# Kernel tuning notes

Hardware: AMD Instinct MI355X
Metric: run time of the kernel (lower is better)

The kernel has to match this reference:

```python
import jax, jax.numpy as jnp
import numpy as np

D_MODEL = 1024
NUM_HEADS = 16
D_K = D_MODEL // NUM_HEADS
B, S = 2, 2048


def setup_inputs() -> dict:
    key = jax.random.key(0)
    ks = jax.random.split(key, 11)
    s = 1.0 / np.sqrt(D_MODEL)
    inp = {
        "Q": jax.random.normal(ks[0], (B, S, D_MODEL), jnp.float32),
        "K": jax.random.normal(ks[1], (B, S, D_MODEL), jnp.float32),
        "V": jax.random.normal(ks[2], (B, S, D_MODEL), jnp.float32),
        "Wq": jax.random.uniform(ks[3], (D_MODEL, D_MODEL), jnp.float32, -s, s),
        "bq": jax.random.uniform(ks[4], (D_MODEL,), jnp.float32, -s, s),
        "Wk": jax.random.uniform(ks[5], (D_MODEL, D_MODEL), jnp.float32, -s, s),
        "bk": jax.random.uniform(ks[6], (D_MODEL,), jnp.float32, -s, s),
        "Wv": jax.random.uniform(ks[7], (D_MODEL, D_MODEL), jnp.float32, -s, s),
        "bv": jax.random.uniform(ks[8], (D_MODEL,), jnp.float32, -s, s),
        "Wo": jax.random.uniform(ks[9], (D_MODEL, D_MODEL), jnp.float32, -s, s),
        "bo": jax.random.uniform(ks[10], (D_MODEL,), jnp.float32, -s, s),
    }
    return inp


def _split_heads(x):
    b, s, _ = x.shape
    return x.reshape(b, s, NUM_HEADS, D_K).transpose(0, 2, 1, 3)  # [B,H,S,Dk]


def reference(Q, K, V, Wq, bq, Wk, bk, Wv, bv, Wo, bo):
    q = _split_heads(Q @ Wq.T + bq)
    k = _split_heads(K @ Wk.T + bk)
    v = _split_heads(V @ Wv.T + bv)
    scale = 1.0 / jnp.sqrt(jnp.asarray(D_K, q.dtype))
    scores = jnp.einsum("bhqd,bhkd->bhqk", q, k) * scale  # [B,H,S,S]
    attn = jax.nn.softmax(scores, axis=-1)
    out = jnp.einsum("bhqk,bhkd->bhqd", attn, v)
    out = out.transpose(0, 2, 1, 3).reshape(Q.shape[0], -1, D_MODEL)
    return out @ Wo.T + bo
```

## Files before the change

kernel.cpp:

```cpp
#include <hip/hip_runtime.h>
#include <stdint.h>

typedef __bf16 bf16;
typedef __bf16 bf16x8 __attribute__((ext_vector_type(8)));
typedef float floatx4 __attribute__((ext_vector_type(4)));

#define S_LEN 2048
#define DM 1024
#define NH 16
#define DK 64
#define MTOT 4096

__device__ __forceinline__ void gll16(const void* g, void* l) {
  __builtin_amdgcn_global_load_lds(
      (const __attribute__((address_space(1))) void*)g,
      (__attribute__((address_space(3))) void*)l, 16, 0, 0);
}

__global__ __launch_bounds__(256) void cvt_w_kernel(
    const float* __restrict__ Wq, const float* __restrict__ Wk, const float* __restrict__ Wv,
    bf16* __restrict__ wqb, bf16* __restrict__ wkb, bf16* __restrict__ wvb)
{
  const int z = blockIdx.y;
  const float* src = (z == 0) ? Wq : (z == 1) ? Wk : Wv;
  bf16* dst = (z == 0) ? wqb : (z == 1) ? wkb : wvb;
  const int base = (blockIdx.x * 256 + threadIdx.x) * 8;
  float4 a = *(const float4*)(src + base);
  float4 b = *(const float4*)(src + base + 4);
  bf16x8 h;
  h[0] = (bf16)a.x; h[1] = (bf16)a.y; h[2] = (bf16)a.z; h[3] = (bf16)a.w;
  h[4] = (bf16)b.x; h[5] = (bf16)b.y; h[6] = (bf16)b.z; h[7] = (bf16)b.w;
  *(bf16x8*)(dst + base) = h;
}

__global__ __launch_bounds__(256) void proj_kernel(
    const float* __restrict__ Xq, const float* __restrict__ Xk, const float* __restrict__ Xv,
    const bf16* __restrict__ wqb, const bf16* __restrict__ wkb, const bf16* __restrict__ wvb,
    const float* __restrict__ bqp, const float* __restrict__ bkp, const float* __restrict__ bvp,
    bf16* __restrict__ qb, bf16* __restrict__ kb, bf16* __restrict__ vtb)
{
  const int z = blockIdx.z;
  const float* X    = (z == 0) ? Xq  : (z == 1) ? Xk  : Xv;
  const bf16* W     = (z == 0) ? wqb : (z == 1) ? wkb : wvb;
  const float* bias = (z == 0) ? bqp : (z == 1) ? bkp : bvp;

  const int m0 = blockIdx.x * 128;
  const int n0 = blockIdx.y * 128;
  const int tid = threadIdx.x;
  const int lane = tid & 63;
  const int wid = tid >> 6;
  const int wm = (wid & 1) * 64;
  const int wn = (wid >> 1) * 64;

  __shared__ float Asf[128 * 64];
  __shared__ bf16  Bs[128 * 64];

  floatx4 acc[4][4];
  #pragma unroll
  for (int i = 0; i < 4; i++)
    #pragma unroll
    for (int j = 0; j < 4; j++) acc[i][j] = (floatx4){0.f, 0.f, 0.f, 0.f};

  const int mr = lane & 15;
  const int q4 = lane >> 4;

  const int xrow_in = lane >> 4;
  const int xcb_ph  = lane & 15;
  const int wrow_in = lane >> 3;
  const int wcb_ph  = lane & 7;

  for (int kt = 0; kt < DM; kt += 64) {
    __syncthreads();
    #pragma unroll
    for (int j = 0; j < 8; j++) {
      const int c = wid * 8 + j;
      const int row = c * 4 + xrow_in;
      const int cb = xcb_ph ^ (row & 7);
      gll16(X + (size_t)(m0 + row) * DM + kt + cb * 4, &Asf[c * 256]);
    }
    #pragma unroll
    for (int j = 0; j < 4; j++) {
      const int c = wid * 4 + j;
      const int row = c * 8 + wrow_in;
      const int cb = wcb_ph ^ (row & 7);
      gll16(W + (size_t)(n0 + row) * DM + kt + cb * 8, &Bs[c * 512]);
    }
    __syncthreads();

    #pragma unroll
    for (int kk = 0; kk < 2; kk++) {
      bf16x8 af[4], bfr[4];
      #pragma unroll
      for (int mt = 0; mt < 4; mt++) {
        const int row = wm + mt * 16 + mr;
        const int cb0 = 8 * kk + 2 * q4;
        const float4 lo = *(const float4*)&Asf[row * 64 + (cb0 ^ (row & 7)) * 4];
        const float4 hi = *(const float4*)&Asf[row * 64 + ((cb0 + 1) ^ (row & 7)) * 4];
        bf16x8 a;
        a[0] = (bf16)lo.x; a[1] = (bf16)lo.y; a[2] = (bf16)lo.z; a[3] = (bf16)lo.w;
        a[4] = (bf16)hi.x; a[5] = (bf16)hi.y; a[6] = (bf16)hi.z; a[7] = (bf16)hi.w;
        af[mt] = a;
      }
      #pragma unroll
      for (int nt = 0; nt < 4; nt++) {
        const int row = wn + nt * 16 + mr;
        const int cb = 4 * kk + q4;
        bfr[nt] = *(const bf16x8*)&Bs[row * 64 + (cb ^ (row & 7)) * 8];
      }
      #pragma unroll
      for (int mt = 0; mt < 4; mt++)
        #pragma unroll
        for (int nt = 0; nt < 4; nt++)
          acc[mt][nt] = __builtin_amdgcn_mfma_f32_16x16x32_bf16(af[mt], bfr[nt], acc[mt][nt], 0, 0, 0);
    }
  }

  const float qscale = (z == 0) ? 0.125f : 1.0f;
  #pragma unroll
  for (int nt = 0; nt < 4; nt++) {
    const int gn = n0 + wn + nt * 16 + mr;
    const float bv = bias[gn];
    const int h = gn >> 6, d = gn & 63;
    #pragma unroll
    for (int mt = 0; mt < 4; mt++) {
      const int mbase = m0 + wm + mt * 16 + q4 * 4;
      #pragma unroll
      for (int r = 0; r < 4; r++) {
        const int gm = mbase + r;
        const int bi = gm >> 11, s = gm & 2047;
        const bf16 hv = (bf16)((acc[mt][nt][r] + bv) * qscale);
        if (z == 2) {
          vtb[(((size_t)(bi * NH + h)) * DK + d) * S_LEN + s] = hv;
        } else if (z == 0) {
          qb[(((size_t)(bi * NH + h)) * S_LEN + s) * DK + d] = hv;
        } else {
          kb[(((size_t)(bi * NH + h)) * S_LEN + s) * DK + d] = hv;
        }
      }
    }
  }
}

__global__ __launch_bounds__(256) void attn_kernel(
    const bf16* __restrict__ qb, const bf16* __restrict__ kb,
    const bf16* __restrict__ vtb, bf16* __restrict__ ob)
{
  const int qt = blockIdx.x;
  const int bh = blockIdx.y;
  const int tid = threadIdx.x;
  const int lane = tid & 63;
  const int wid = tid >> 6;

  const bf16* qh = qb + (size_t)bh * S_LEN * DK;
  const bf16* kh = kb + (size_t)bh * S_LEN * DK;
  const bf16* vh = vtb + (size_t)bh * DK * S_LEN;

  __shared__ bf16 Ks[128 * 64];
  __shared__ bf16 Vs[64 * 128];
  __shared__ bf16 Ps[4][16][136];

  const int mr = lane & 15;
  const int q4 = lane >> 4;
  const int k0 = q4 * 8;

  bf16x8 aq[2];
  #pragma unroll
  for (int kk = 0; kk < 2; kk++)
    aq[kk] = *(const bf16x8*)(qh + (size_t)(qt * 64 + wid * 16 + mr) * DK + kk * 32 + k0);

  floatx4 acc_o[4];
  #pragma unroll
  for (int i = 0; i < 4; i++) acc_o[i] = (floatx4){0.f, 0.f, 0.f, 0.f};
  float l_p[4] = {0.f, 0.f, 0.f, 0.f};

  const int krow_in = lane >> 3;
  const int kcb_ph  = lane & 7;
  const int vrow_in = lane >> 4;
  const int vcb_ph  = lane & 15;

  for (int it = 0; it < S_LEN / 128; it++) {
    const int s0 = it * 128;
    __syncthreads();
    #pragma unroll
    for (int j = 0; j < 4; j++) {
      const int c = wid * 4 + j;
      const int row = c * 8 + krow_in;
      const int cb = kcb_ph ^ (row & 7);
      gll16(kh + (size_t)(s0 + row) * DK + cb * 8, &Ks[c * 512]);
    }
    #pragma unroll
    for (int j = 0; j < 4; j++) {
      const int c = wid * 4 + j;
      const int row = c * 4 + vrow_in;
      const int cb = vcb_ph ^ (row & 7);
      gll16(vh + (size_t)row * S_LEN + s0 + cb * 8, &Vs[c * 512]);
    }
    __syncthreads();

    floatx4 sc[8];
    #pragma unroll
    for (int i = 0; i < 8; i++) sc[i] = (floatx4){0.f, 0.f, 0.f, 0.f};
    #pragma unroll
    for (int kk = 0; kk < 2; kk++) {
      #pragma unroll
      for (int nt = 0; nt < 8; nt++) {
        const int row = nt * 16 + mr;
        const int cb = kk * 4 + q4;
        bf16x8 b = *(const bf16x8*)&Ks[row * 64 + (cb ^ (row & 7)) * 8];
        sc[nt] = __builtin_amdgcn_mfma_f32_16x16x32_bf16(aq[kk], b, sc[nt], 0, 0, 0);
      }
    }

    #pragma unroll
    for (int nt = 0; nt < 8; nt++) {
      #pragma unroll
      for (int r = 0; r < 4; r++) {
        const float pv = __expf(sc[nt][r]);
        l_p[r] += pv;
        Ps[wid][q4 * 4 + r][nt * 16 + mr] = (bf16)pv;
      }
    }

    #pragma unroll
    for (int kk2 = 0; kk2 < 4; kk2++) {
      bf16x8 a = *(const bf16x8*)&Ps[wid][mr][kk2 * 32 + k0];
      #pragma unroll
      for (int dt = 0; dt < 4; dt++) {
        const int row = dt * 16 + mr;
        const int cb = kk2 * 4 + q4;
        bf16x8 b = *(const bf16x8*)&Vs[row * 128 + (cb ^ (row & 7)) * 8];
        acc_o[dt] = __builtin_amdgcn_mfma_f32_16x16x32_bf16(a, b, acc_o[dt], 0, 0, 0);
      }
    }
  }

  #pragma unroll
  for (int r = 0; r < 4; r++) {
    #pragma unroll
    for (int off = 1; off < 16; off <<= 1) l_p[r] += __shfl_xor(l_p[r], off, 16);
    l_p[r] = 1.0f / l_p[r];
  }

  const int bi = bh >> 4, h = bh & 15;
  #pragma unroll
  for (int dt = 0; dt < 4; dt++) {
    const int d = dt * 16 + mr;
    #pragma unroll
    for (int r = 0; r < 4; r++) {
      const int s = qt * 64 + wid * 16 + q4 * 4 + r;
      ob[((size_t)(bi * S_LEN + s)) * DM + h * DK + d] = (bf16)(acc_o[dt][r] * l_p[r]);
    }
  }
}

__global__ __launch_bounds__(256) void oproj_kernel(
    const bf16* __restrict__ X, const float* __restrict__ W,
    const float* __restrict__ bias, float* __restrict__ out)
{
  const int m0 = blockIdx.x * 128;
  const int n0 = blockIdx.y * 128;
  const int tid = threadIdx.x;
  const int lane = tid & 63;
  const int wid = tid >> 6;
  const int wm = (wid & 1) * 64;
  const int wn = (wid >> 1) * 64;

  __shared__ bf16  As[128 * 64];
  __shared__ float Bsf[128 * 64];

  floatx4 acc[4][4];
  #pragma unroll
  for (int i = 0; i < 4; i++)
    #pragma unroll
    for (int j = 0; j < 4; j++) acc[i][j] = (floatx4){0.f, 0.f, 0.f, 0.f};

  const int mr = lane & 15;
  const int q4 = lane >> 4;

  const int arow_in = lane >> 3;
  const int acb_ph  = lane & 7;
  const int brow_in = lane >> 4;
  const int bcb_ph  = lane & 15;

  for (int kt = 0; kt < DM; kt += 64) {
    __syncthreads();
    #pragma unroll
    for (int j = 0; j < 4; j++) {
      const int c = wid * 4 + j;
      const int row = c * 8 + arow_in;
      const int cb = acb_ph ^ (row & 7);
      gll16(X + (size_t)(m0 + row) * DM + kt + cb * 8, &As[c * 512]);
    }
    #pragma unroll
    for (int j = 0; j < 8; j++) {
      const int c = wid * 8 + j;
      const int row = c * 4 + brow_in;
      const int cb = bcb_ph ^ (row & 7);
      gll16(W + (size_t)(n0 + row) * DM + kt + cb * 4, &Bsf[c * 256]);
    }
    __syncthreads();

    #pragma unroll
    for (int kk = 0; kk < 2; kk++) {
      bf16x8 af[4], bfr[4];
      #pragma unroll
      for (int mt = 0; mt < 4; mt++) {
        const int row = wm + mt * 16 + mr;
        const int cb = 4 * kk + q4;
        af[mt] = *(const bf16x8*)&As[row * 64 + (cb ^ (row & 7)) * 8];
      }
      #pragma unroll
      for (int nt = 0; nt < 4; nt++) {
        const int row = wn + nt * 16 + mr;
        const int cb0 = 8 * kk + 2 * q4;
        const float4 lo = *(const float4*)&Bsf[row * 64 + (cb0 ^ (row & 7)) * 4];
        const float4 hi = *(const float4*)&Bsf[row * 64 + ((cb0 + 1) ^ (row & 7)) * 4];
        bf16x8 b;
        b[0] = (bf16)lo.x; b[1] = (bf16)lo.y; b[2] = (bf16)lo.z; b[3] = (bf16)lo.w;
        b[4] = (bf16)hi.x; b[5] = (bf16)hi.y; b[6] = (bf16)hi.z; b[7] = (bf16)hi.w;
        bfr[nt] = b;
      }
      #pragma unroll
      for (int mt = 0; mt < 4; mt++)
        #pragma unroll
        for (int nt = 0; nt < 4; nt++)
          acc[mt][nt] = __builtin_amdgcn_mfma_f32_16x16x32_bf16(af[mt], bfr[nt], acc[mt][nt], 0, 0, 0);
    }
  }

  #pragma unroll
  for (int nt = 0; nt < 4; nt++) {
    const int gn = n0 + wn + nt * 16 + mr;
    const float bv = bias[gn];
    #pragma unroll
    for (int mt = 0; mt < 4; mt++) {
      const int mbase = m0 + wm + mt * 16 + q4 * 4;
      #pragma unroll
      for (int r = 0; r < 4; r++)
        out[(size_t)(mbase + r) * DM + gn] = acc[mt][nt][r] + bv;
    }
  }
}

extern "C" void kernel_launch(void* const* d_in, const int* in_sizes, int n_in,
                              void* d_out, int out_size, void* d_ws, size_t ws_size,
                              hipStream_t stream) {
  const float* Q  = (const float*)d_in[0];
  const float* K  = (const float*)d_in[1];
  const float* V  = (const float*)d_in[2];
  const float* Wq = (const float*)d_in[3];
  const float* bq = (const float*)d_in[4];
  const float* Wk = (const float*)d_in[5];
  const float* bk = (const float*)d_in[6];
  const float* Wv = (const float*)d_in[7];
  const float* bv = (const float*)d_in[8];
  const float* Wo = (const float*)d_in[9];
  const float* bo = (const float*)d_in[10];
  float* out = (float*)d_out;

  const size_t NE = (size_t)MTOT * DM;
  bf16* qb  = (bf16*)d_ws;
  bf16* kb  = qb + NE;
  bf16* vtb = kb + NE;
  bf16* ao  = vtb + NE;
  bf16* wqb = ao;
  bf16* wkb = ao + (size_t)DM * DM;
  bf16* wvb = ao + 2 * (size_t)DM * DM;

  cvt_w_kernel<<<dim3(512, 3), 256, 0, stream>>>(Wq, Wk, Wv, wqb, wkb, wvb);
  proj_kernel<<<dim3(32, 8, 3), 256, 0, stream>>>(Q, K, V, wqb, wkb, wvb, bq, bk, bv, qb, kb, vtb);
  attn_kernel<<<dim3(32, 32), 256, 0, stream>>>(qb, kb, vtb, ao);
  oproj_kernel<<<dim3(32, 8), 256, 0, stream>>>(ao, Wo, bo, out);
}
```

Measured before the change: 282.8 us.

## Pre-convert Q/K inputs to bf16, double attention rows per warp, narrow oproj tiles

The conversion kernel now also casts the Q and K activations to bf16, staging them in the output buffer, so the Q and K projections load bf16 tiles instead of converting fp32 in LDS. The attention kernel now has each warp handle 32 query rows instead of 16, reusing each K and V LDS fragment for two MFMAs and halving the grid. The output projection uses 128x64 tiles, doubling its block count for better occupancy. The extra conversion pass adds global traffic, and the attention change raises register and LDS pressure.

```diff
diff --git a/kernel.cpp b/kernel.cpp
--- a/kernel.cpp
+++ b/kernel.cpp
@@ -17,14 +17,20 @@
       (__attribute__((address_space(3))) void*)l, 16, 0, 0);
 }
 
-__global__ __launch_bounds__(256) void cvt_w_kernel(
+__global__ __launch_bounds__(256) void cvt_kernel(
     const float* __restrict__ Wq, const float* __restrict__ Wk, const float* __restrict__ Wv,
-    bf16* __restrict__ wqb, bf16* __restrict__ wkb, bf16* __restrict__ wvb)
+    const float* __restrict__ Xq, const float* __restrict__ Xk,
+    bf16* __restrict__ wqb, bf16* __restrict__ wkb, bf16* __restrict__ wvb,
+    bf16* __restrict__ xqb, bf16* __restrict__ xkb)
 {
-  const int z = blockIdx.y;
-  const float* src = (z == 0) ? Wq : (z == 1) ? Wk : Wv;
-  bf16* dst = (z == 0) ? wqb : (z == 1) ? wkb : wvb;
-  const int base = (blockIdx.x * 256 + threadIdx.x) * 8;
+  const int c = blockIdx.x;
+  const float* src; bf16* dst; int off;
+  if      (c < 512)  { src = Wq; dst = wqb; off = c; }
+  else if (c < 1024) { src = Wk; dst = wkb; off = c - 512; }
+  else if (c < 1536) { src = Wv; dst = wvb; off = c - 1024; }
+  else if (c < 3584) { src = Xq; dst = xqb; off = c - 1536; }
+  else               { src = Xk; dst = xkb; off = c - 3584; }
+  const size_t base = (size_t)off * 2048 + threadIdx.x * 8;
   float4 a = *(const float4*)(src + base);
   float4 b = *(const float4*)(src + base + 4);
   bf16x8 h;
@@ -34,13 +40,12 @@
 }
 
 __global__ __launch_bounds__(256) void proj_kernel(
-    const float* __restrict__ Xq, const float* __restrict__ Xk, const float* __restrict__ Xv,
+    const bf16* __restrict__ xqb, const bf16* __restrict__ xkb, const float* __restrict__ Xv,
     const bf16* __restrict__ wqb, const bf16* __restrict__ wkb, const bf16* __restrict__ wvb,
     const float* __restrict__ bqp, const float* __restrict__ bkp, const float* __restrict__ bvp,
     bf16* __restrict__ qb, bf16* __restrict__ kb, bf16* __restrict__ vtb)
 {
   const int z = blockIdx.z;
-  const float* X    = (z == 0) ? Xq  : (z == 1) ? Xk  : Xv;
   const bf16* W     = (z == 0) ? wqb : (z == 1) ? wkb : wvb;
   const float* bias = (z == 0) ? bqp : (z == 1) ? bkp : bvp;
 
@@ -52,8 +57,10 @@
   const int wm = (wid & 1) * 64;
   const int wn = (wid >> 1) * 64;
 
-  __shared__ float Asf[128 * 64];
-  __shared__ bf16  Bs[128 * 64];
+  __shared__ unsigned char smemA[32768];
+  __shared__ bf16 Bs[128 * 64];
+  bf16*  As16 = (bf16*)smemA;
+  float* Asf  = (float*)smemA;
 
   floatx4 acc[4][4];
   #pragma unroll
@@ -64,25 +71,35 @@
   const int mr = lane & 15;
   const int q4 = lane >> 4;
 
-  const int xrow_in = lane >> 4;
-  const int xcb_ph  = lane & 15;
-  const int wrow_in = lane >> 3;
-  const int wcb_ph  = lane & 7;
+  const int r8_in = lane >> 3, cb8_ph = lane & 7;
+  const int r4_in = lane >> 4, cb16_ph = lane & 15;
+
+  const bf16* Xb = (z == 0) ? xqb : xkb;
 
   for (int kt = 0; kt < DM; kt += 64) {
     __syncthreads();
-    #pragma unroll
-    for (int j = 0; j < 8; j++) {
-      const int c = wid * 8 + j;
-      const int row = c * 4 + xrow_in;
-      const int cb = xcb_ph ^ (row & 7);
-      gll16(X + (size_t)(m0 + row) * DM + kt + cb * 4, &Asf[c * 256]);
+    if (z < 2) {
+      #pragma unroll
+      for (int j = 0; j < 4; j++) {
+        const int c = wid * 4 + j;
+        const int row = c * 8 + r8_in;
+        const int cb = cb8_ph ^ (row & 7);
+        gll16(Xb + (size_t)(m0 + row) * DM + kt + cb * 8, &As16[c * 512]);
+      }
+    } else {
+      #pragma unroll
+      for (int j = 0; j < 8; j++) {
+        const int c = wid * 8 + j;
+        const int row = c * 4 + r4_in;
+        const int cb = cb16_ph ^ (row & 7);
+        gll16(Xv + (size_t)(m0 + row) * DM + kt + cb * 4, &Asf[c * 256]);
+      }
     }
     #pragma unroll
     for (int j = 0; j < 4; j++) {
       const int c = wid * 4 + j;
-      const int row = c * 8 + wrow_in;
-      const int cb = wcb_ph ^ (row & 7);
+      const int row = c * 8 + r8_in;
+      const int cb = cb8_ph ^ (row & 7);
       gll16(W + (size_t)(n0 + row) * DM + kt + cb * 8, &Bs[c * 512]);
     }
     __syncthreads();
@@ -93,13 +110,18 @@
       #pragma unroll
       for (int mt = 0; mt < 4; mt++) {
         const int row = wm + mt * 16 + mr;
-        const int cb0 = 8 * kk + 2 * q4;
-        const float4 lo = *(const float4*)&Asf[row * 64 + (cb0 ^ (row & 7)) * 4];
-        const float4 hi = *(const float4*)&Asf[row * 64 + ((cb0 + 1) ^ (row & 7)) * 4];
-        bf16x8 a;
-        a[0] = (bf16)lo.x; a[1] = (bf16)lo.y; a[2] = (bf16)lo.z; a[3] = (bf16)lo.w;
-        a[4] = (bf16)hi.x; a[5] = (bf16)hi.y; a[6] = (bf16)hi.z; a[7] = (bf16)hi.w;
-        af[mt] = a;
+        if (z < 2) {
+          const int cb = 4 * kk + q4;
+          af[mt] = *(const bf16x8*)&As16[row * 64 + (cb ^ (row & 7)) * 8];
+        } else {
+          const int cb0 = 8 * kk + 2 * q4;
+          const float4 lo = *(const float4*)&Asf[row * 64 + (cb0 ^ (row & 7)) * 4];
+          const float4 hi = *(const float4*)&Asf[row * 64 + ((cb0 + 1) ^ (row & 7)) * 4];
+          bf16x8 a;
+          a[0] = (bf16)lo.x; a[1] = (bf16)lo.y; a[2] = (bf16)lo.z; a[3] = (bf16)lo.w;
+          a[4] = (bf16)hi.x; a[5] = (bf16)hi.y; a[6] = (bf16)hi.z; a[7] = (bf16)hi.w;
+          af[mt] = a;
+        }
       }
       #pragma unroll
       for (int nt = 0; nt < 4; nt++) {
@@ -157,26 +179,27 @@
 
   __shared__ bf16 Ks[128 * 64];
   __shared__ bf16 Vs[64 * 128];
-  __shared__ bf16 Ps[4][16][136];
+  __shared__ bf16 Ps[4][32][136];
 
   const int mr = lane & 15;
   const int q4 = lane >> 4;
-  const int k0 = q4 * 8;
-
-  bf16x8 aq[2];
-  #pragma unroll
-  for (int kk = 0; kk < 2; kk++)
-    aq[kk] = *(const bf16x8*)(qh + (size_t)(qt * 64 + wid * 16 + mr) * DK + kk * 32 + k0);
-
-  floatx4 acc_o[4];
-  #pragma unroll
-  for (int i = 0; i < 4; i++) acc_o[i] = (floatx4){0.f, 0.f, 0.f, 0.f};
-  float l_p[4] = {0.f, 0.f, 0.f, 0.f};
-
-  const int krow_in = lane >> 3;
-  const int kcb_ph  = lane & 7;
-  const int vrow_in = lane >> 4;
-  const int vcb_ph  = lane & 15;
+
+  bf16x8 aq[2][2];
+  #pragma unroll
+  for (int mt = 0; mt < 2; mt++)
+    #pragma unroll
+    for (int kk = 0; kk < 2; kk++)
+      aq[mt][kk] = *(const bf16x8*)(qh + (size_t)(qt * 128 + wid * 32 + mt * 16 + mr) * DK + kk * 32 + q4 * 8);
+
+  floatx4 acc_o[2][4];
+  #pragma unroll
+  for (int mt = 0; mt < 2; mt++)
+    #pragma unroll
+    for (int dt = 0; dt < 4; dt++) acc_o[mt][dt] = (floatx4){0.f, 0.f, 0.f, 0.f};
+  float l_p[2][4] = {{0.f,0.f,0.f,0.f},{0.f,0.f,0.f,0.f}};
+
+  const int r8_in = lane >> 3, cb8_ph = lane & 7;
+  const int r4_in = lane >> 4, cb16_ph = lane & 15;
 
   for (int it = 0; it < S_LEN / 128; it++) {
     const int s0 = it * 128;
@@ -184,22 +207,24 @@
     #pragma unroll
     for (int j = 0; j < 4; j++) {
       const int c = wid * 4 + j;
-      const int row = c * 8 + krow_in;
-      const int cb = kcb_ph ^ (row & 7);
+      const int row = c * 8 + r8_in;
+      const int cb = cb8_ph ^ (row & 7);
       gll16(kh + (size_t)(s0 + row) * DK + cb * 8, &Ks[c * 512]);
     }
     #pragma unroll
     for (int j = 0; j < 4; j++) {
       const int c = wid * 4 + j;
-      const int row = c * 4 + vrow_in;
-      const int cb = vcb_ph ^ (row & 7);
+      const int row = c * 4 + r4_in;
+      const int cb = cb16_ph ^ (row & 7);
       gll16(vh + (size_t)row * S_LEN + s0 + cb * 8, &Vs[c * 512]);
     }
     __syncthreads();
 
-    floatx4 sc[8];
-    #pragma unroll
-    for (int i = 0; i < 8; i++) sc[i] = (floatx4){0.f, 0.f, 0.f, 0.f};
+    floatx4 sc[2][8];
+    #pragma unroll
+    for (int mt = 0; mt < 2; mt++)
+      #pragma unroll
+      for (int i = 0; i < 8; i++) sc[mt][i] = (floatx4){0.f, 0.f, 0.f, 0.f};
     #pragma unroll
     for (int kk = 0; kk < 2; kk++) {
       #pragma unroll
@@ -207,48 +232,60 @@
         const int row = nt * 16 + mr;
         const int cb = kk * 4 + q4;
         bf16x8 b = *(const bf16x8*)&Ks[row * 64 + (cb ^ (row & 7)) * 8];
-        sc[nt] = __builtin_amdgcn_mfma_f32_16x16x32_bf16(aq[kk], b, sc[nt], 0, 0, 0);
-      }
-    }
-
-    #pragma unroll
-    for (int nt = 0; nt < 8; nt++) {
-      #pragma unroll
-      for (int r = 0; r < 4; r++) {
-        const float pv = __expf(sc[nt][r]);
-        l_p[r] += pv;
-        Ps[wid][q4 * 4 + r][nt * 16 + mr] = (bf16)pv;
-      }
-    }
+        #pragma unroll
+        for (int mt = 0; mt < 2; mt++)
+          sc[mt][nt] = __builtin_amdgcn_mfma_f32_16x16x32_bf16(aq[mt][kk], b, sc[mt][nt], 0, 0, 0);
+      }
+    }
+
+    #pragma unroll
+    for (int mt = 0; mt < 2; mt++)
+      #pragma unroll
+      for (int nt = 0; nt < 8; nt++)
+        #pragma unroll
+        for (int r = 0; r < 4; r++) {
+          const float pv = __expf(sc[mt][nt][r]);
+          l_p[mt][r] += pv;
+          Ps[wid][mt * 16 + q4 * 4 + r][nt * 16 + mr] = (bf16)pv;
+        }
 
     #pragma unroll
     for (int kk2 = 0; kk2 < 4; kk2++) {
-      bf16x8 a = *(const bf16x8*)&Ps[wid][mr][kk2 * 32 + k0];
+      bf16x8 ap[2];
+      #pragma unroll
+      for (int mt = 0; mt < 2; mt++)
+        ap[mt] = *(const bf16x8*)&Ps[wid][mt * 16 + mr][kk2 * 32 + q4 * 8];
       #pragma unroll
       for (int dt = 0; dt < 4; dt++) {
         const int row = dt * 16 + mr;
         const int cb = kk2 * 4 + q4;
         bf16x8 b = *(const bf16x8*)&Vs[row * 128 + (cb ^ (row & 7)) * 8];
-        acc_o[dt] = __builtin_amdgcn_mfma_f32_16x16x32_bf16(a, b, acc_o[dt], 0, 0, 0);
-      }
-    }
-  }
-
-  #pragma unroll
-  for (int r = 0; r < 4; r++) {
-    #pragma unroll
-    for (int off = 1; off < 16; off <<= 1) l_p[r] += __shfl_xor(l_p[r], off, 16);
-    l_p[r] = 1.0f / l_p[r];
+        #pragma unroll
+        for (int mt = 0; mt < 2; mt++)
+          acc_o[mt][dt] = __builtin_amdgcn_mfma_f32_16x16x32_bf16(ap[mt], b, acc_o[mt][dt], 0, 0, 0);
+      }
+    }
   }
 
   const int bi = bh >> 4, h = bh & 15;
   #pragma unroll
-  for (int dt = 0; dt < 4; dt++) {
-    const int d = dt * 16 + mr;
+  for (int mt = 0; mt < 2; mt++) {
+    float inv[4];
     #pragma unroll
     for (int r = 0; r < 4; r++) {
-      const int s = qt * 64 + wid * 16 + q4 * 4 + r;
-      ob[((size_t)(bi * S_LEN + s)) * DM + h * DK + d] = (bf16)(acc_o[dt][r] * l_p[r]);
+      float v = l_p[mt][r];
+      #pragma unroll
+      for (int off = 1; off < 16; off <<= 1) v += __shfl_xor(v, off, 16);
+      inv[r] = 1.0f / v;
+    }
+    #pragma unroll
+    for (int dt = 0; dt < 4; dt++) {
+      const int d = dt * 16 + mr;
+      #pragma unroll
+      for (int r = 0; r < 4; r++) {
+        const int s = qt * 128 + wid * 32 + mt * 16 + q4 * 4 + r;
+        ob[((size_t)(bi * S_LEN + s)) * DM + h * DK + d] = (bf16)(acc_o[mt][dt][r] * inv[r]);
+      }
     }
   }
 }
@@ -258,60 +295,57 @@
     const float* __restrict__ bias, float* __restrict__ out)
 {
   const int m0 = blockIdx.x * 128;
-  const int n0 = blockIdx.y * 128;
+  const int n0 = blockIdx.y * 64;
   const int tid = threadIdx.x;
   const int lane = tid & 63;
   const int wid = tid >> 6;
-  const int wm = (wid & 1) * 64;
-  const int wn = (wid >> 1) * 64;
+  const int wm = wid * 32;
 
   __shared__ bf16  As[128 * 64];
-  __shared__ float Bsf[128 * 64];
-
-  floatx4 acc[4][4];
-  #pragma unroll
-  for (int i = 0; i < 4; i++)
+  __shared__ float Bsf[64 * 64];
+
+  floatx4 acc[2][4];
+  #pragma unroll
+  for (int i = 0; i < 2; i++)
     #pragma unroll
     for (int j = 0; j < 4; j++) acc[i][j] = (floatx4){0.f, 0.f, 0.f, 0.f};
 
   const int mr = lane & 15;
   const int q4 = lane >> 4;
 
-  const int arow_in = lane >> 3;
-  const int acb_ph  = lane & 7;
-  const int brow_in = lane >> 4;
-  const int bcb_ph  = lane & 15;
+  const int r8_in = lane >> 3, cb8_ph = lane & 7;
+  const int r4_in = lane >> 4, cb16_ph = lane & 15;
 
   for (int kt = 0; kt < DM; kt += 64) {
     __syncthreads();
     #pragma unroll
     for (int j = 0; j < 4; j++) {
       const int c = wid * 4 + j;
-      const int row = c * 8 + arow_in;
-      const int cb = acb_ph ^ (row & 7);
+      const int row = c * 8 + r8_in;
+      const int cb = cb8_ph ^ (row & 7);
       gll16(X + (size_t)(m0 + row) * DM + kt + cb * 8, &As[c * 512]);
     }
     #pragma unroll
-    for (int j = 0; j < 8; j++) {
-      const int c = wid * 8 + j;
-      const int row = c * 4 + brow_in;
-      const int cb = bcb_ph ^ (row & 7);
+    for (int j = 0; j < 4; j++) {
+      const int c = wid * 4 + j;
+      const int row = c * 4 + r4_in;
+      const int cb = cb16_ph ^ (row & 7);
       gll16(W + (size_t)(n0 + row) * DM + kt + cb * 4, &Bsf[c * 256]);
     }
     __syncthreads();
 
     #pragma unroll
     for (int kk = 0; kk < 2; kk++) {
-      bf16x8 af[4], bfr[4];
-      #pragma unroll
-      for (int mt = 0; mt < 4; mt++) {
+      bf16x8 af[2], bfr[4];
+      #pragma unroll
+      for (int mt = 0; mt < 2; mt++) {
         const int row = wm + mt * 16 + mr;
         const int cb = 4 * kk + q4;
         af[mt] = *(const bf16x8*)&As[row * 64 + (cb ^ (row & 7)) * 8];
       }
       #pragma unroll
       for (int nt = 0; nt < 4; nt++) {
-        const int row = wn + nt * 16 + mr;
+        const int row = nt * 16 + mr;
         const int cb0 = 8 * kk + 2 * q4;
         const float4 lo = *(const float4*)&Bsf[row * 64 + (cb0 ^ (row & 7)) * 4];
         const float4 hi = *(const float4*)&Bsf[row * 64 + ((cb0 + 1) ^ (row & 7)) * 4];
@@ -321,7 +355,7 @@
         bfr[nt] = b;
       }
       #pragma unroll
-      for (int mt = 0; mt < 4; mt++)
+      for (int mt = 0; mt < 2; mt++)
         #pragma unroll
         for (int nt = 0; nt < 4; nt++)
           acc[mt][nt] = __builtin_amdgcn_mfma_f32_16x16x32_bf16(af[mt], bfr[nt], acc[mt][nt], 0, 0, 0);
@@ -330,10 +364,10 @@
 
   #pragma unroll
   for (int nt = 0; nt < 4; nt++) {
-    const int gn = n0 + wn + nt * 16 + mr;
+    const int gn = n0 + nt * 16 + mr;
     const float bv = bias[gn];
     #pragma unroll
-    for (int mt = 0; mt < 4; mt++) {
+    for (int mt = 0; mt < 2; mt++) {
       const int mbase = m0 + wm + mt * 16 + q4 * 4;
       #pragma unroll
       for (int r = 0; r < 4; r++)
@@ -366,9 +400,11 @@
   bf16* wqb = ao;
   bf16* wkb = ao + (size_t)DM * DM;
   bf16* wvb = ao + 2 * (size_t)DM * DM;
-
-  cvt_w_kernel<<<dim3(512, 3), 256, 0, stream>>>(Wq, Wk, Wv, wqb, wkb, wvb);
-  proj_kernel<<<dim3(32, 8, 3), 256, 0, stream>>>(Q, K, V, wqb, wkb, wvb, bq, bk, bv, qb, kb, vtb);
-  attn_kernel<<<dim3(32, 32), 256, 0, stream>>>(qb, kb, vtb, ao);
-  oproj_kernel<<<dim3(32, 8), 256, 0, stream>>>(ao, Wo, bo, out);
-}
+  bf16* xqb = (bf16*)d_out;
+  bf16* xkb = xqb + NE;
+
+  cvt_kernel<<<dim3(5632), 256, 0, stream>>>(Wq, Wk, Wv, Q, K, wqb, wkb, wvb, xqb, xkb);
+  proj_kernel<<<dim3(32, 8, 3), 256, 0, stream>>>(xqb, xkb, V, wqb, wkb, wvb, bq, bk, bv, qb, kb, vtb);
+  attn_kernel<<<dim3(16, 32), 256, 0, stream>>>(qb, kb, vtb, ao);
+  oproj_kernel<<<dim3(32, 16), 256, 0, stream>>>(ao, Wo, bo, out);
+}
```

New measurement: 262.8 us. 1.08x faster.
